# Performance work log

Measured on AMD Instinct MI355X. Metric: run time of the kernel, lower is better.

The kernel has to match this reference:

```python
import jax, jax.numpy as jnp
import numpy as np

_EPS = 1e-5

def _bn(x, g, t, m, v):
    # inference-mode BatchNorm (channels-last)
    return g * (x - m) * jax.lax.rsqrt(v + _EPS) + t

def _lin(x, w, b):
    # 1x1 conv == linear over last (channel) axis; w: (out, in)
    return jnp.einsum('...c,oc->...o', x, w) + b

def _forward(points, k, c0_w, c0_b, c0_g, c0_t, c0_m, c0_v,
             c1_w, c1_b, c1_g, c1_t, c1_m, c1_v,
             a0_w, a0_b, a0_g, a0_t, a0_m, a0_v,
             a1_w, a1_b, a1_g, a1_t, a1_m, a1_v,
             a2_w, a2_b, a2_g, a2_t, a2_m, a2_v,
             c2_w, c2_b, c2_g, c2_t, c2_m, c2_v,
             c3_w, c3_b, c3_g, c3_t, c3_m, c3_v,
             c4_w, c4_b):
    B, N, _ = points.shape
    # per-point MLP: 3 -> 64 -> 64
    x = jax.nn.relu(_bn(_lin(points, c0_w, c0_b), c0_g, c0_t, c0_m, c0_v))
    x = jax.nn.relu(_bn(_lin(x, c1_w, c1_b), c1_g, c1_t, c1_m, c1_v))
    # kNN via squared distances (same ordering as cdist); idx: (B,N,k)
    sq = jnp.sum(points * points, axis=-1)  # (B,N)
    d = sq[:, :, None] + sq[:, None, :] - 2.0 * jnp.einsum('bnc,bmc->bnm', points, points)
    idx = jax.lax.top_k(-d, k)[1]  # (B,N,k) smallest distances
    bidx = jnp.arange(B)[:, None, None]
    grouped_xyz = points[bidx, idx] - points[:, :, None, :]  # (B,N,k,3), centered
    grouped_pts = x[bidx, idx]                                # (B,N,k,64)
    g = jnp.concatenate([grouped_xyz, grouped_pts], axis=-1)  # (B,N,k,67)
    # per-neighbor MLP 67 -> 64 -> 128 -> 128
    for (w, b, ga, t, m, v) in ((a0_w, a0_b, a0_g, a0_t, a0_m, a0_v),
                                (a1_w, a1_b, a1_g, a1_t, a1_m, a1_v),
                                (a2_w, a2_b, a2_g, a2_t, a2_m, a2_v)):
        g = jax.nn.relu(_bn(_lin(g, w, b), ga, t, m, v))
    local = jnp.max(g, axis=2)                 # (B,N,128) max over k neighbors
    gf = jnp.max(local, axis=1, keepdims=True)  # (B,1,128) global feature
    feat = jnp.concatenate([local, jnp.broadcast_to(gf, local.shape)], axis=-1)  # (B,N,256)
    feat = jax.nn.relu(_bn(_lin(feat, c2_w, c2_b), c2_g, c2_t, c2_m, c2_v))
    feat = jax.nn.relu(_bn(_lin(feat, c3_w, c3_b), c3_g, c3_t, c3_m, c3_v))
    # dropout is identity in eval mode
    return _lin(feat, c4_w, c4_b)  # (B,N,6)

def setup_inputs() -> dict:
    key = jax.random.key(0)
    B, N, K = 8, 4096, 16
    specs = [("c0", 64, 3, True), ("c1", 64, 64, True), ("a0", 64, 67, True),
             ("a1", 128, 64, True), ("a2", 128, 128, True), ("c2", 256, 256, True),
             ("c3", 128, 256, True), ("c4", 6, 128, False)]
    inp = {"points": jax.random.normal(key, (B, N, 3), jnp.float32)}
    i = 0
    for name, o, c, has_bn in specs:
        i += 1
        kw = jax.random.fold_in(key, i)
        inp[name + "_w"] = jax.random.normal(kw, (o, c), jnp.float32) * 0.05
        inp[name + "_b"] = jnp.zeros((o,), jnp.float32)
        if has_bn:
            inp[name + "_g"] = jnp.ones((o,), jnp.float32)
            inp[name + "_t"] = jnp.zeros((o,), jnp.float32)
            inp[name + "_m"] = jax.random.normal(jax.random.fold_in(kw, 1), (o,), jnp.float32) * 0.05
            inp[name + "_v"] = jnp.ones((o,), jnp.float32)
    inp["k"] = K
    return inp

def reference(points, c0_w, c0_b, c0_g, c0_t, c0_m, c0_v,
              c1_w, c1_b, c1_g, c1_t, c1_m, c1_v,
              a0_w, a0_b, a0_g, a0_t, a0_m, a0_v,
              a1_w, a1_b, a1_g, a1_t, a1_m, a1_v,
              a2_w, a2_b, a2_g, a2_t, a2_m, a2_v,
              c2_w, c2_b, c2_g, c2_t, c2_m, c2_v,
              c3_w, c3_b, c3_g, c3_t, c3_m, c3_v,
              c4_w, c4_b, k):
    return _forward(points, k, c0_w, c0_b, c0_g, c0_t, c0_m, c0_v,
                    c1_w, c1_b, c1_g, c1_t, c1_m, c1_v,
                    a0_w, a0_b, a0_g, a0_t, a0_m, a0_v,
                    a1_w, a1_b, a1_g, a1_t, a1_m, a1_v,
                    a2_w, a2_b, a2_g, a2_t, a2_m, a2_v,
                    c2_w, c2_b, c2_g, c2_t, c2_m, c2_v,
                    c3_w, c3_b, c3_g, c3_t, c3_m, c3_v,
                    c4_w, c4_b)
```

## Files before the change

### kernel.cpp

```cpp
#include <hip/hip_runtime.h>
#include <math.h>


#define EPSBN 1e-5f

typedef _Float16 v8h  __attribute__((ext_vector_type(8)));
typedef _Float16 v4h  __attribute__((ext_vector_type(4)));
typedef float    v16f __attribute__((ext_vector_type(16)));

#define W0T_OFF   0
#define B0_OFF    192
#define W1T_OFF   256
#define B1_OFF    4352
#define A0XT_OFF  4416
#define A0FT_OFF  4608
#define BA0_OFF   8704
#define A1T_OFF   8768
#define BA1_OFF   16960
#define A2T_OFF   17088
#define BA2_OFF   33472
#define C2T_OFF   33600
#define C3H_OFF   66368
#define BC2_OFF   99136
#define BC3_OFF   132160
#define C4T_OFF   132288
#define BC4_OFF   133056
#define PTS4_OFF  133120
#define Q_OFF     264192
#define C_OFF     2361344
#define IDX_OFF   4458496
#define LOCAL_OFF 4982784
#define GF_OFF    9177088

__device__ __forceinline__ void fold_one(int e, const float* w, const float* b,
    const float* g, const float* t, const float* m, const float* v,
    float* wt, float* bo, int O, int Cfull, int cbeg)
{
    int o = e % O, c = e / O;
    float s = 1.0f;
    if (g) s = g[o] * (1.0f / sqrtf(v[o] + EPSBN));
    wt[c * O + o] = w[o * Cfull + cbeg + c] * s;
    if (c == 0 && bo) {
        float bias = b[o];
        if (g) bias = (bias - m[o]) * s + t[o];
        bo[o] = bias;
    }
}

__global__ __launch_bounds__(256) void fold_kernel(
    const float* c0w, const float* c0b, const float* c0g, const float* c0t, const float* c0m, const float* c0v,
    const float* c1w, const float* c1b, const float* c1g, const float* c1t, const float* c1m, const float* c1v,
    const float* a0w, const float* a0b, const float* a0g, const float* a0t, const float* a0m, const float* a0v,
    const float* a1w, const float* a1b, const float* a1g, const float* a1t, const float* a1m, const float* a1v,
    const float* a2w, const float* a2b, const float* a2g, const float* a2t, const float* a2m, const float* a2v,
    const float* c2w, const float* c2b, const float* c2g, const float* c2t, const float* c2m, const float* c2v,
    const float* c3w, const float* c3b, const float* c3g, const float* c3t, const float* c3m, const float* c3v,
    const float* c4w, const float* c4b,
    float* ws)
{
    int e = blockIdx.x * 256 + threadIdx.x;
    if (e < 192)        { fold_one(e,          c0w, c0b, c0g, c0t, c0m, c0v, ws + W0T_OFF,  ws + B0_OFF,  64, 3,   0); return; }
    e -= 192;
    if (e < 4096)       { fold_one(e,          c1w, c1b, c1g, c1t, c1m, c1v, ws + W1T_OFF,  ws + B1_OFF,  64, 64,  0); return; }
    e -= 4096;
    if (e < 192)        { fold_one(e,          a0w, a0b, a0g, a0t, a0m, a0v, ws + A0XT_OFF, ws + BA0_OFF, 64, 67,  0); return; }
    e -= 192;
    if (e < 4096)       { fold_one(e,          a0w, a0b, a0g, a0t, a0m, a0v, ws + A0FT_OFF, nullptr,      64, 67,  3); return; }
    e -= 4096;
    if (e < 8192) {
        int j = e & 7, l = (e >> 3) & 63, kf = (e >> 9) & 3, wv = e >> 11;
        int o = wv * 32 + (l & 31);
        int c = kf * 16 + (l >> 5) * 8 + j;
        float s = a1g[o] * (1.0f / sqrtf(a1v[o] + EPSBN));
        ((_Float16*)(ws + A1T_OFF))[e] = (_Float16)(a1w[o * 64 + c] * s);
        if (c == 0) ws[BA1_OFF + o] = (a1b[o] - a1m[o]) * s + a1t[o];
        return;
    }
    e -= 8192;
    if (e < 16384) {
        int j = e & 7, l = (e >> 3) & 63, kf = (e >> 9) & 7, wv = e >> 12;
        int o = wv * 32 + (l & 31);
        int c = kf * 16 + (l >> 5) * 8 + j;
        float s = a2g[o] * (1.0f / sqrtf(a2v[o] + EPSBN));
        ((_Float16*)(ws + A2T_OFF))[e] = (_Float16)(a2w[o * 128 + c] * s);
        if (c == 0) ws[BA2_OFF + o] = (a2b[o] - a2m[o]) * s + a2t[o];
        return;
    }
    e -= 16384;
    if (e < 65536) {
        int j = e & 7, l = (e >> 3) & 63, s5 = (e >> 9) & 15, ot = e >> 13;
        int o = ot * 32 + (l & 31);
        int c = s5 * 16 + (l >> 5) * 8 + j;
        float sc = c2g[o] * (1.0f / sqrtf(c2v[o] + EPSBN));
        ((_Float16*)(ws + C2T_OFF))[e] = (_Float16)(c2w[o * 256 + c] * sc);
        if (c == 0) ws[BC2_OFF + o] = (c2b[o] - c2m[o]) * sc + c2t[o];
        return;
    }
    e -= 65536;
    if (e < 32768) {
        int j = e & 7, l = (e >> 3) & 63, s5 = (e >> 9) & 15, ot = e >> 13;
        int o = ot * 32 + (l & 31);
        int c = s5 * 16 + (l >> 5) * 8 + j;
        float sc = c3g[o] * (1.0f / sqrtf(c3v[o] + EPSBN));
        ((_Float16*)(ws + C3H_OFF))[e] = (_Float16)(c3w[o * 256 + c] * sc);
        if (c == 0) ws[BC3_OFF + o] = (c3b[o] - c3m[o]) * sc + c3t[o];
        return;
    }
    e -= 32768;
    if (e < 768)        { fold_one(e,          c4w, c4b, nullptr, nullptr, nullptr, nullptr, ws + C4T_OFF, ws + BC4_OFF, 6, 128, 0); return; }
    e -= 768;
    if (e < 1024)       { ws[GF_OFF + e] = 0.0f; return; }
}

__global__ __launch_bounds__(256) void point_mlp_kernel(const float* __restrict__ pts, float* __restrict__ ws)
{
    __shared__ float sh[4][64][4];
    __shared__ float sx[4][64][4];
    int lane = threadIdx.x & 63;
    int wv = threadIdx.x >> 6;
    int pid0 = blockIdx.x * 16 + wv * 4;

    const float* pc = pts + (size_t)pid0 * 3;
    float c0x = pc[0], c0y = pc[1],  c0z = pc[2];
    float c1x = pc[3], c1y = pc[4],  c1z = pc[5];
    float c2x = pc[6], c2y = pc[7],  c2z = pc[8];
    float c3x = pc[9], c3y = pc[10], c3z = pc[11];

    if (lane < 4) {
        const float* pp = pts + (size_t)(pid0 + lane) * 3;
        float xx = pp[0], yy = pp[1], zz = pp[2];
        float sq = __fadd_rn(__fadd_rn(__fmul_rn(xx, xx), __fmul_rn(yy, yy)), __fmul_rn(zz, zz));
        ((float4*)(ws + PTS4_OFF))[pid0 + lane] = make_float4(xx, yy, zz, sq);
    }

    const float* W0T  = ws + W0T_OFF;
    const float* B0   = ws + B0_OFF;
    const float* W1T  = ws + W1T_OFF;
    const float* B1   = ws + B1_OFF;
    const float* A0XT = ws + A0XT_OFF;
    const float* A0FT = ws + A0FT_OFF;
    const float* BA0  = ws + BA0_OFF;

    float b0 = B0[lane];
    float w0a = W0T[lane], w0b = W0T[64 + lane], w0c = W0T[128 + lane];
    float4 h;
    h.x = fmaxf(fmaf(c0z, w0c, fmaf(c0y, w0b, fmaf(c0x, w0a, b0))), 0.0f);
    h.y = fmaxf(fmaf(c1z, w0c, fmaf(c1y, w0b, fmaf(c1x, w0a, b0))), 0.0f);
    h.z = fmaxf(fmaf(c2z, w0c, fmaf(c2y, w0b, fmaf(c2x, w0a, b0))), 0.0f);
    h.w = fmaxf(fmaf(c3z, w0c, fmaf(c3y, w0b, fmaf(c3x, w0a, b0))), 0.0f);
    *(float4*)&sh[wv][lane][0] = h;

    float b1v = B1[lane];
    float a0 = b1v, a1 = b1v, a2 = b1v, a3 = b1v;
    #pragma unroll 8
    for (int c = 0; c < 64; ++c) {
        float w = W1T[c * 64 + lane];
        float4 hv = *(const float4*)&sh[wv][c][0];
        a0 = fmaf(w, hv.x, a0);
        a1 = fmaf(w, hv.y, a1);
        a2 = fmaf(w, hv.z, a2);
        a3 = fmaf(w, hv.w, a3);
    }
    float4 xv;
    xv.x = fmaxf(a0, 0.0f);
    xv.y = fmaxf(a1, 0.0f);
    xv.z = fmaxf(a2, 0.0f);
    xv.w = fmaxf(a3, 0.0f);
    *(float4*)&sx[wv][lane][0] = xv;

    float ax = A0XT[lane], ay = A0XT[64 + lane], az = A0XT[128 + lane];
    float q0 = __fmul_rn(c0x, ax); q0 = fmaf(c0y, ay, q0); q0 = fmaf(c0z, az, q0);
    float q1 = __fmul_rn(c1x, ax); q1 = fmaf(c1y, ay, q1); q1 = fmaf(c1z, az, q1);
    float q2 = __fmul_rn(c2x, ax); q2 = fmaf(c2y, ay, q2); q2 = fmaf(c2z, az, q2);
    float q3 = __fmul_rn(c3x, ax); q3 = fmaf(c3y, ay, q3); q3 = fmaf(c3z, az, q3);
    ws[Q_OFF + (size_t)(pid0 + 0) * 64 + lane] = q0;
    ws[Q_OFF + (size_t)(pid0 + 1) * 64 + lane] = q1;
    ws[Q_OFF + (size_t)(pid0 + 2) * 64 + lane] = q2;
    ws[Q_OFF + (size_t)(pid0 + 3) * 64 + lane] = q3;

    float ba = BA0[lane];
    float e0 = q0 + ba, e1 = q1 + ba, e2 = q2 + ba, e3 = q3 + ba;
    #pragma unroll 8
    for (int c = 0; c < 64; ++c) {
        float w = A0FT[c * 64 + lane];
        float4 sv = *(const float4*)&sx[wv][c][0];
        e0 = fmaf(w, sv.x, e0);
        e1 = fmaf(w, sv.y, e1);
        e2 = fmaf(w, sv.z, e2);
        e3 = fmaf(w, sv.w, e3);
    }
    ws[C_OFF + (size_t)(pid0 + 0) * 64 + lane] = e0;
    ws[C_OFF + (size_t)(pid0 + 1) * 64 + lane] = e1;
    ws[C_OFF + (size_t)(pid0 + 2) * 64 + lane] = e2;
    ws[C_OFF + (size_t)(pid0 + 3) * 64 + lane] = e3;
}

__device__ __forceinline__ float dist2_ref(float xn, float yn, float zn, float sqn, float4 pm)
{
    float dot = __fmul_rn(xn, pm.x);
    dot = __fmaf_rn(yn, pm.y, dot);
    dot = __fmaf_rn(zn, pm.z, dot);
    float s = __fadd_rn(sqn, pm.w);
    return __fmaf_rn(-2.0f, dot, s);
}

__device__ __forceinline__ float dtilde(float xn, float yn, float zn, float4 pm)
{
    float dot = __fmul_rn(xn, pm.x);
    dot = __fmaf_rn(yn, pm.y, dot);
    dot = __fmaf_rn(zn, pm.z, dot);
    return __fmaf_rn(-2.0f, dot, pm.w);
}

#define KNN_CAP 64
#define KNN_MARGIN 1e-3f

__device__ __forceinline__ void knn_row(
    const float4* __restrict__ pts4, int* __restrict__ IDX,
    float* __restrict__ bufdW, int* __restrict__ bufiW, int* __restrict__ cntp,
    int base, int rbase, int rw, int l, float gm, float tvd)
{
    unsigned long long qm = __ballot(gm <= tvd);

    float4 pr = pts4[rbase + rw];
    float xr = pr.x, yr = pr.y, zr = pr.z, sr = pr.w;
    float tve = __fadd_rn(sr, tvd);

    int cr = 0;
    #define KNN_PROC(GG, CV)                                                   \
    {                                                                          \
        float d = dist2_ref(xr, yr, zr, sr, (CV));                             \
        bool p = (d <= tve);                                                   \
        unsigned long long mk = __ballot(p);                                   \
        int my = __builtin_amdgcn_mbcnt_hi((unsigned)(mk >> 32),               \
                 __builtin_amdgcn_mbcnt_lo((unsigned)mk, 0));                  \
        int slot = cr + my;                                                    \
        if (p && slot < KNN_CAP) { bufdW[slot] = d; bufiW[slot] = (GG) * 64 + l; } \
        cr += (int)__popcll(mk);                                               \
    }
    while (qm) {
        int g0 = __ffsll((unsigned long long)qm) - 1; qm &= qm - 1;
        int g1 = -1, g2 = -1, g3 = -1;
        if (qm) { g1 = __ffsll((unsigned long long)qm) - 1; qm &= qm - 1;
            if (qm) { g2 = __ffsll((unsigned long long)qm) - 1; qm &= qm - 1;
                if (qm) { g3 = __ffsll((unsigned long long)qm) - 1; qm &= qm - 1; } } }
        float4 cv0 = pts4[base + g0 * 64 + l];
        float4 cv1, cv2, cv3;
        if (g1 >= 0) cv1 = pts4[base + g1 * 64 + l];
        if (g2 >= 0) cv2 = pts4[base + g2 * 64 + l];
        if (g3 >= 0) cv3 = pts4[base + g3 * 64 + l];
        KNN_PROC(g0, cv0);
        if (g1 >= 0) KNN_PROC(g1, cv1);
        if (g2 >= 0) KNN_PROC(g2, cv2);
        if (g3 >= 0) KNN_PROC(g3, cv3);
    }
    #undef KNN_PROC
    if (l == 0) *cntp = cr;

    if (cr <= KNN_CAP) {
        unsigned long long key = ~0ULL;
        if (l < cr) {
            unsigned u = __float_as_uint(bufdW[l]);
            u = (u & 0x80000000u) ? ~u : (u | 0x80000000u);
            key = ((unsigned long long)u << 32) | (unsigned)bufiW[l];
        }
        if (cr <= 32) {
            #pragma unroll
            for (int k = 2; k <= 32; k <<= 1) {
                #pragma unroll
                for (int j = k >> 1; j > 0; j >>= 1) {
                    unsigned long long o = __shfl_xor(key, j);
                    bool mx = (((l & j) != 0) == ((l & k) == 0));
                    key = mx ? (key > o ? key : o) : (key < o ? key : o);
                }
            }
        } else {
            #pragma unroll
            for (int k = 2; k <= 64; k <<= 1) {
                #pragma unroll
                for (int j = k >> 1; j > 0; j >>= 1) {
                    unsigned long long o = __shfl_xor(key, j);
                    bool mx = (((l & j) != 0) == ((l & k) == 0));
                    key = mx ? (key > o ? key : o) : (key < o ? key : o);
                }
            }
        }
        if (l < 16)
            IDX[(rbase + rw) * 16 + l] = (int)(key & 0xFFFFFFFFu);
    }
}

__global__ __launch_bounds__(1024) void knn_kernel(float* __restrict__ ws)
{
    __shared__ float gmins[64 * 65];
    __shared__ float bufd[16][72];
    __shared__ int   bufi[16][72];
    __shared__ int   cnt[64];

    const float4* __restrict__ pts4 = (const float4*)(ws + PTS4_OFF);
    int* IDX = (int*)(ws + IDX_OFF);

    const int l     = threadIdx.x & 63;
    const int row   = l;
    const int wvu   = __builtin_amdgcn_readfirstlane(threadIdx.x >> 6);
    const int base  = (blockIdx.x >> 6) << 12;
    const int rbase = blockIdx.x * 64;
    const int r     = rbase + row;

    float4 pn = pts4[r];
    float xn = pn.x, yn = pn.y, zn = pn.z;

    #pragma unroll
    for (int g = 0; g < 4; ++g) {
        const float4* __restrict__ cp = pts4 + base + wvu * 256 + g * 64;
        float mn0 = INFINITY, mn1 = INFINITY, mn2 = INFINITY, mn3 = INFINITY;
        #pragma unroll 4
        for (int i = 0; i < 64; i += 4) {
            mn0 = fminf(mn0, dtilde(xn, yn, zn, cp[i + 0]));
            mn1 = fminf(mn1, dtilde(xn, yn, zn, cp[i + 1]));
            mn2 = fminf(mn2, dtilde(xn, yn, zn, cp[i + 2]));
            mn3 = fminf(mn3, dtilde(xn, yn, zn, cp[i + 3]));
        }
        gmins[row * 65 + wvu * 4 + g] = fminf(fminf(mn0, mn1), fminf(mn2, mn3));
    }
    __syncthreads();

    float gm0 = gmins[(wvu * 4 + 0) * 65 + l];
    float gm1 = gmins[(wvu * 4 + 1) * 65 + l];
    float gm2 = gmins[(wvu * 4 + 2) * 65 + l];
    float gm3 = gmins[(wvu * 4 + 3) * 65 + l];
    float v0 = gm0, v1 = gm1, v2 = gm2, v3 = gm3;
    #pragma unroll
    for (int k = 2; k <= 64; k <<= 1) {
        #pragma unroll
        for (int j = k >> 1; j > 0; j >>= 1) {
            float o0 = __shfl_xor(v0, j);
            float o1 = __shfl_xor(v1, j);
            float o2 = __shfl_xor(v2, j);
            float o3 = __shfl_xor(v3, j);
            bool mx = (((l & j) != 0) == ((l & k) == 0));
            v0 = mx ? fmaxf(v0, o0) : fminf(v0, o0);
            v1 = mx ? fmaxf(v1, o1) : fminf(v1, o1);
            v2 = mx ? fmaxf(v2, o2) : fminf(v2, o2);
            v3 = mx ? fmaxf(v3, o3) : fminf(v3, o3);
        }
    }
    float tvd0 = __shfl(v0, 16) + KNN_MARGIN;
    float tvd1 = __shfl(v1, 16) + KNN_MARGIN;
    float tvd2 = __shfl(v2, 16) + KNN_MARGIN;
    float tvd3 = __shfl(v3, 16) + KNN_MARGIN;

    knn_row(pts4, IDX, bufd[wvu], bufi[wvu], &cnt[wvu * 4 + 0], base, rbase, wvu * 4 + 0, l, gm0, tvd0);
    knn_row(pts4, IDX, bufd[wvu], bufi[wvu], &cnt[wvu * 4 + 1], base, rbase, wvu * 4 + 1, l, gm1, tvd1);
    knn_row(pts4, IDX, bufd[wvu], bufi[wvu], &cnt[wvu * 4 + 2], base, rbase, wvu * 4 + 2, l, gm2, tvd2);
    knn_row(pts4, IDX, bufd[wvu], bufi[wvu], &cnt[wvu * 4 + 3], base, rbase, wvu * 4 + 3, l, gm3, tvd3);
    __syncthreads();

    if (threadIdx.x < 64 && cnt[threadIdx.x] > KNN_CAP) {
        int* out = IDX + (rbase + threadIdx.x) * 16;
        float4 pq = pts4[rbase + threadIdx.x];
        float hd[16]; int hi[16];
        #pragma unroll
        for (int t2 = 0; t2 < 16; ++t2) { hd[t2] = INFINITY; hi[t2] = 0; }
        for (int mm = 0; mm < 4096; ++mm) {
            float d = dist2_ref(pq.x, pq.y, pq.z, pq.w, pts4[base + mm]);
            if (d < hd[15]) {
                float vd = d; int vi = mm;
                #pragma unroll
                for (int t2 = 0; t2 < 16; ++t2) {
                    bool sm = vd < hd[t2];
                    float td = hd[t2]; int ti = hi[t2];
                    if (sm) { hd[t2] = vd; hi[t2] = vi; vd = td; vi = ti; }
                }
            }
        }
        for (int jj = 0; jj < 16; ++jj) out[jj] = hi[jj];
    }
}

__device__ __forceinline__ void nbr_stage_g1(
    _Float16* sG1, const float* Cf, const float* Qf,
    int t, int gpt0, int g, int base, int m)
{
    int r = t >> 2, cs = t & 3;
    int gpt = gpt0 + g * 4 + (r >> 4);
    const float4* crow = (const float4*)(Cf + (size_t)(base + m) * 64) + cs * 4;
    const float4* qrow = (const float4*)(Qf + (size_t)gpt * 64) + cs * 4;
    v8h h0, h1;
    #pragma unroll
    for (int u = 0; u < 2; ++u) {
        float4 cv = crow[u], qv = qrow[u];
        h0[u * 4 + 0] = (_Float16)fmaxf(cv.x - qv.x, 0.0f);
        h0[u * 4 + 1] = (_Float16)fmaxf(cv.y - qv.y, 0.0f);
        h0[u * 4 + 2] = (_Float16)fmaxf(cv.z - qv.z, 0.0f);
        h0[u * 4 + 3] = (_Float16)fmaxf(cv.w - qv.w, 0.0f);
    }
    #pragma unroll
    for (int u = 0; u < 2; ++u) {
        float4 cv = crow[2 + u], qv = qrow[2 + u];
        h1[u * 4 + 0] = (_Float16)fmaxf(cv.x - qv.x, 0.0f);
        h1[u * 4 + 1] = (_Float16)fmaxf(cv.y - qv.y, 0.0f);
        h1[u * 4 + 2] = (_Float16)fmaxf(cv.z - qv.z, 0.0f);
        h1[u * 4 + 3] = (_Float16)fmaxf(cv.w - qv.w, 0.0f);
    }
    int rs = r & 7;
    *(v8h*)&sG1[r * 64 + ((cs * 2    ) ^ rs) * 8] = h0;
    *(v8h*)&sG1[r * 64 + ((cs * 2 + 1) ^ rs) * 8] = h1;
}

__global__ __launch_bounds__(256) void nbr_mlp_mfma_kernel(float* __restrict__ ws)
{
    __shared__ __align__(16) unsigned char smem[33280];
    _Float16* sG1   = (_Float16*)smem;
    _Float16* sH1   = (_Float16*)(smem + 8192);
    float*    sPool = (float*)(smem + 24576);
    float*    sB1   = (float*)(smem + 32768);

    const int t   = threadIdx.x;
    const int l   = t & 63;
    const int w   = t >> 6;
    const int ln  = l & 31;
    const int hi  = l >> 5;
    const int blk = blockIdx.x;
    const int gpt0 = blk * 16;
    const int base = (blk >> 8) << 12;

    const float* Cf = ws + C_OFF;
    const float* Qf = ws + Q_OFF;
    const int* IDX = (const int*)(ws + IDX_OFF);

    if (t < 128) sB1[t] = ws[BA1_OFF + t];
    float b2ch = ws[BA2_OFF + w * 32 + ln];

    int mi[4];
    {
        int r = t >> 2;
        #pragma unroll
        for (int g = 0; g < 4; ++g)
            mi[g] = IDX[(gpt0 + g * 4 + (r >> 4)) * 16 + (r & 15)];
    }

    v8h fa[4], fa2[8];
    {
        const float4* a1img = (const float4*)(ws + A1T_OFF);
        const float4* a2img = (const float4*)(ws + A2T_OFF);
        #pragma unroll
        for (int kf = 0; kf < 4; ++kf) {
            float4 tmp = a1img[(w * 4 + kf) * 64 + l];
            fa[kf] = *(v8h*)&tmp;
        }
        #pragma unroll
        for (int kf = 0; kf < 8; ++kf) {
            float4 tmp = a2img[(w * 8 + kf) * 64 + l];
            fa2[kf] = *(v8h*)&tmp;
        }
    }

    nbr_stage_g1(sG1, Cf, Qf, t, gpt0, 0, base, mi[0]);
    __syncthreads();

    for (int g = 0; g < 4; ++g) {
        #pragma unroll
        for (int rt = 0; rt < 2; ++rt) {
            int r = rt * 32 + ln, rs = r & 7;
            v16f acc;
            #pragma unroll
            for (int i = 0; i < 16; ++i) acc[i] = 0.0f;
            #pragma unroll
            for (int kf = 0; kf < 4; ++kf) {
                v8h fb = *(const v8h*)&sG1[r * 64 + ((kf * 2 + hi) ^ rs) * 8];
                acc = __builtin_amdgcn_mfma_f32_32x32x16_f16(fa[kf], fb, acc, 0, 0, 0);
            }
            #pragma unroll
            for (int q = 0; q < 4; ++q) {
                float4 b4 = *(const float4*)&sB1[w * 32 + 8 * q + 4 * hi];
                v4h hv;
                hv[0] = (_Float16)fmaxf(acc[q * 4 + 0] + b4.x, 0.0f);
                hv[1] = (_Float16)fmaxf(acc[q * 4 + 1] + b4.y, 0.0f);
                hv[2] = (_Float16)fmaxf(acc[q * 4 + 2] + b4.z, 0.0f);
                hv[3] = (_Float16)fmaxf(acc[q * 4 + 3] + b4.w, 0.0f);
                int gg = w * 4 + q;
                *(v4h*)&sH1[r * 128 + ((gg ^ rs) * 8) + 4 * hi] = hv;
            }
        }
        __syncthreads();

        if (g < 3) nbr_stage_g1(sG1, Cf, Qf, t, gpt0, g + 1, base, mi[g + 1]);

        #pragma unroll
        for (int rt = 0; rt < 2; ++rt) {
            int r = rt * 32 + ln, rs = r & 7;
            v16f acc;
            #pragma unroll
            for (int i = 0; i < 16; ++i) acc[i] = 0.0f;
            #pragma unroll
            for (int kf = 0; kf < 8; ++kf) {
                v8h fb = *(const v8h*)&sH1[r * 128 + ((kf * 2 + hi) ^ rs) * 8];
                acc = __builtin_amdgcn_mfma_f32_32x32x16_f16(fb, fa2[kf], acc, 0, 0, 0);
            }
            float p0 = acc[0], p1 = acc[8];
            #pragma unroll
            for (int i = 1; i < 8; ++i) { p0 = fmaxf(p0, acc[i]); p1 = fmaxf(p1, acc[8 + i]); }
            p0 = fmaxf(p0, __shfl_xor(p0, 32));
            p1 = fmaxf(p1, __shfl_xor(p1, 32));
            float o0 = fmaxf(p0 + b2ch, 0.0f);
            float o1 = fmaxf(p1 + b2ch, 0.0f);
            if (hi == 0) {
                int p = g * 4 + rt * 2;
                sPool[p * 128 + w * 32 + ln]       = o0;
                sPool[(p + 1) * 128 + w * 32 + ln] = o1;
            }
        }
        __syncthreads();
    }

    {
        float* LOCAL = ws + LOCAL_OFF;
        const float4* sp4 = (const float4*)sPool;
        #pragma unroll
        for (int u = 0; u < 2; ++u) {
            int e = t + 256 * u;
            int pp = e >> 5, cc = e & 31;
            ((float4*)&LOCAL[(size_t)(gpt0 + pp) * 128])[cc] = sp4[e];
        }
    }

    if (t < 128) {
        float m = 0.0f;
        #pragma unroll
        for (int p = 0; p < 16; ++p) m = fmaxf(m, sPool[p * 128 + t]);
        atomicMax((int*)(ws + GF_OFF) + (blk >> 8) * 128 + t, __float_as_int(m));
    }
}

__global__ __launch_bounds__(256) void head_mfma_kernel(float* __restrict__ ws, float* __restrict__ out)
{
    __shared__ __align__(16) unsigned char smem[66560];
    _Float16* sF  = (_Float16*)smem;
    float*    sF3 = (float*)smem;
    _Float16* sF2 = (_Float16*)(smem + 33792);

    const int t  = threadIdx.x;
    const int l  = t & 63;
    const int w  = t >> 6;
    const int ln = l & 31;
    const int hi = l >> 5;
    const int gpt0 = blockIdx.x * 64;
    const int b = blockIdx.x >> 6;

    const float4* c2h = (const float4*)(ws + C2T_OFF);
    const float4* c3h = (const float4*)(ws + C3H_OFF);

    {
        int m = t >> 2, cs = t & 3;
        const float4* src = (cs < 2)
            ? (const float4*)(ws + LOCAL_OFF + (size_t)(gpt0 + m) * 128) + cs * 16
            : (const float4*)(ws + GF_OFF + b * 128) + (cs - 2) * 16;
        int c0 = cs * 64;
        #pragma unroll
        for (int u = 0; u < 8; ++u) {
            float4 a0 = src[u * 2], a1 = src[u * 2 + 1];
            v8h h;
            h[0] = (_Float16)a0.x; h[1] = (_Float16)a0.y;
            h[2] = (_Float16)a0.z; h[3] = (_Float16)a0.w;
            h[4] = (_Float16)a1.x; h[5] = (_Float16)a1.y;
            h[6] = (_Float16)a1.z; h[7] = (_Float16)a1.w;
            int g = ((c0 >> 3) + u) ^ (m & 31);
            *(v8h*)&sF[m * 256 + g * 8] = h;
        }
    }
    __syncthreads();

    #pragma unroll
    for (int ot = 0; ot < 2; ++ot) {
        int ot2 = 2 * w + ot;
        v8h fa[16];
        #pragma unroll
        for (int s = 0; s < 16; ++s) {
            float4 tmp = c2h[(ot2 * 16 + s) * 64 + l];
            fa[s] = *(v8h*)&tmp;
        }
        float b2[16];
        #pragma unroll
        for (int i = 0; i < 16; ++i)
            b2[i] = ws[BC2_OFF + ot2 * 32 + (i & 3) + 8 * (i >> 2) + 4 * hi];
        #pragma unroll
        for (int mt = 0; mt < 2; ++mt) {
            int m = mt * 32 + ln;
            v16f acc;
            #pragma unroll
            for (int i = 0; i < 16; ++i) acc[i] = 0.0f;
            #pragma unroll
            for (int s = 0; s < 16; ++s) {
                v8h fb = *(const v8h*)&sF[m * 256 + (((2 * s + hi) ^ ln) * 8)];
                acc = __builtin_amdgcn_mfma_f32_32x32x16_f16(fa[s], fb, acc, 0, 0, 0);
            }
            #pragma unroll
            for (int q = 0; q < 4; ++q) {
                v4h hv;
                #pragma unroll
                for (int j = 0; j < 4; ++j)
                    hv[j] = (_Float16)fmaxf(acc[q * 4 + j] + b2[q * 4 + j], 0.0f);
                *(v4h*)&sF2[m * 256 + (((ot2 * 4 + q) ^ ln) * 8) + 4 * hi] = hv;
            }
        }
    }
    __syncthreads();

    {
        v8h fa[16];
        #pragma unroll
        for (int s = 0; s < 16; ++s) {
            float4 tmp = c3h[(w * 16 + s) * 64 + l];
            fa[s] = *(v8h*)&tmp;
        }
        float b3[16];
        #pragma unroll
        for (int i = 0; i < 16; ++i)
            b3[i] = ws[BC3_OFF + w * 32 + (i & 3) + 8 * (i >> 2) + 4 * hi];
        #pragma unroll
        for (int mt = 0; mt < 2; ++mt) {
            int m = mt * 32 + ln;
            v16f acc;
            #pragma unroll
            for (int i = 0; i < 16; ++i) acc[i] = 0.0f;
            #pragma unroll
            for (int s = 0; s < 16; ++s) {
                v8h fb = *(const v8h*)&sF2[m * 256 + (((2 * s + hi) ^ ln) * 8)];
                acc = __builtin_amdgcn_mfma_f32_32x32x16_f16(fa[s], fb, acc, 0, 0, 0);
            }
            #pragma unroll
            for (int q = 0; q < 4; ++q) {
                float4 hv;
                hv.x = fmaxf(acc[q * 4 + 0] + b3[q * 4 + 0], 0.0f);
                hv.y = fmaxf(acc[q * 4 + 1] + b3[q * 4 + 1], 0.0f);
                hv.z = fmaxf(acc[q * 4 + 2] + b3[q * 4 + 2], 0.0f);
                hv.w = fmaxf(acc[q * 4 + 3] + b3[q * 4 + 3], 0.0f);
                *(float4*)&sF3[m * 132 + w * 32 + q * 8 + 4 * hi] = hv;
            }
        }
    }
    __syncthreads();

    const float* C4T = ws + C4T_OFF;
    for (int mo = t; mo < 384; mo += 256) {
        int m = mo / 6, o = mo - m * 6;
        float a = ws[BC4_OFF + o];
        const float4* f4 = (const float4*)(sF3 + m * 132);
        #pragma unroll 8
        for (int kq = 0; kq < 32; ++kq) {
            float4 f = f4[kq];
            a = fmaf(f.x, C4T[(kq * 4 + 0) * 6 + o], a);
            a = fmaf(f.y, C4T[(kq * 4 + 1) * 6 + o], a);
            a = fmaf(f.z, C4T[(kq * 4 + 2) * 6 + o], a);
            a = fmaf(f.w, C4T[(kq * 4 + 3) * 6 + o], a);
        }
        out[(size_t)(gpt0 + m) * 6 + o] = a;
    }
}

extern "C" void kernel_launch(void* const* d_in, const int* in_sizes, int n_in,
                              void* d_out, int out_size, void* d_ws, size_t ws_size,
                              hipStream_t stream)
{
    const float* pts = (const float*)d_in[0];
    float* ws = (float*)d_ws;
    float* out = (float*)d_out;

    fold_kernel<<<521, 256, 0, stream>>>(
        (const float*)d_in[1],  (const float*)d_in[2],  (const float*)d_in[3],  (const float*)d_in[4],  (const float*)d_in[5],  (const float*)d_in[6],
        (const float*)d_in[7],  (const float*)d_in[8],  (const float*)d_in[9],  (const float*)d_in[10], (const float*)d_in[11], (const float*)d_in[12],
        (const float*)d_in[13], (const float*)d_in[14], (const float*)d_in[15], (const float*)d_in[16], (const float*)d_in[17], (const float*)d_in[18],
        (const float*)d_in[19], (const float*)d_in[20], (const float*)d_in[21], (const float*)d_in[22], (const float*)d_in[23], (const float*)d_in[24],
        (const float*)d_in[25], (const float*)d_in[26], (const float*)d_in[27], (const float*)d_in[28], (const float*)d_in[29], (const float*)d_in[30],
        (const float*)d_in[31], (const float*)d_in[32], (const float*)d_in[33], (const float*)d_in[34], (const float*)d_in[35], (const float*)d_in[36],
        (const float*)d_in[37], (const float*)d_in[38], (const float*)d_in[39], (const float*)d_in[40], (const float*)d_in[41], (const float*)d_in[42],
        (const float*)d_in[43], (const float*)d_in[44],
        ws);

    point_mlp_kernel<<<2048, 256, 0, stream>>>(pts, ws);
    knn_kernel<<<512, 1024, 0, stream>>>(ws);
    nbr_mlp_mfma_kernel<<<2048, 256, 0, stream>>>(ws);
    head_mfma_kernel<<<512, 256, 0, stream>>>(ws, out);
}
```

Measured before the change: 291.6 us.

## Interleave two kNN rows per wave and widen head kernel to 512 threads

The kNN candidate scan now handles two query rows at once per wave. It interleaves their candidate-group loads and the ballot/compaction steps, and runs both bitonic sorts together, to expose more memory- and instruction-level parallelism. Each row gets its own shared-memory buffer, which increases LDS usage. Separately, the head kernel moves from 256 to 512 threads, giving each wave one output tile per GEMM stage. This gives more waves to hide latency but means less register reuse of weights per wave.

New measurement: 283.5 us, median of 2. 2.8% less time.

```diff
diff --git a/kernel.cpp b/kernel.cpp
--- a/kernel.cpp
+++ b/kernel.cpp
@@ -215,86 +215,100 @@
 #define KNN_CAP 64
 #define KNN_MARGIN 1e-3f
 
-__device__ __forceinline__ void knn_row(
+__device__ __forceinline__ void knn_pair(
     const float4* __restrict__ pts4, int* __restrict__ IDX,
-    float* __restrict__ bufdW, int* __restrict__ bufiW, int* __restrict__ cntp,
-    int base, int rbase, int rw, int l, float gm, float tvd)
-{
-    unsigned long long qm = __ballot(gm <= tvd);
-
-    float4 pr = pts4[rbase + rw];
-    float xr = pr.x, yr = pr.y, zr = pr.z, sr = pr.w;
-    float tve = __fadd_rn(sr, tvd);
-
-    int cr = 0;
-    #define KNN_PROC(GG, CV)                                                   \
+    float* __restrict__ bdA, int* __restrict__ biA,
+    float* __restrict__ bdB, int* __restrict__ biB,
+    int* __restrict__ cntA, int* __restrict__ cntB,
+    int base, int rgA, int rgB, int l,
+    float gmA, float gmB, float tvdA, float tvdB)
+{
+    float4 pA = pts4[rgA];
+    float4 pB = pts4[rgB];
+    float tveA = __fadd_rn(pA.w, tvdA);
+    float tveB = __fadd_rn(pB.w, tvdB);
+    unsigned long long qA = __ballot(gmA <= tvdA);
+    unsigned long long qB = __ballot(gmB <= tvdB);
+    int crA = 0, crB = 0;
+
+    #define KNN_PROC2(GG, CV, PP, TVE, CR, BD, BI)                             \
     {                                                                          \
-        float d = dist2_ref(xr, yr, zr, sr, (CV));                             \
-        bool p = (d <= tve);                                                   \
+        float d = dist2_ref((PP).x, (PP).y, (PP).z, (PP).w, (CV));             \
+        bool p = ((GG) >= 0) & (d <= (TVE));                                   \
         unsigned long long mk = __ballot(p);                                   \
         int my = __builtin_amdgcn_mbcnt_hi((unsigned)(mk >> 32),               \
                  __builtin_amdgcn_mbcnt_lo((unsigned)mk, 0));                  \
-        int slot = cr + my;                                                    \
-        if (p && slot < KNN_CAP) { bufdW[slot] = d; bufiW[slot] = (GG) * 64 + l; } \
-        cr += (int)__popcll(mk);                                               \
-    }
-    while (qm) {
-        int g0 = __ffsll((unsigned long long)qm) - 1; qm &= qm - 1;
-        int g1 = -1, g2 = -1, g3 = -1;
-        if (qm) { g1 = __ffsll((unsigned long long)qm) - 1; qm &= qm - 1;
-            if (qm) { g2 = __ffsll((unsigned long long)qm) - 1; qm &= qm - 1;
-                if (qm) { g3 = __ffsll((unsigned long long)qm) - 1; qm &= qm - 1; } } }
-        float4 cv0 = pts4[base + g0 * 64 + l];
-        float4 cv1, cv2, cv3;
-        if (g1 >= 0) cv1 = pts4[base + g1 * 64 + l];
-        if (g2 >= 0) cv2 = pts4[base + g2 * 64 + l];
-        if (g3 >= 0) cv3 = pts4[base + g3 * 64 + l];
-        KNN_PROC(g0, cv0);
-        if (g1 >= 0) KNN_PROC(g1, cv1);
-        if (g2 >= 0) KNN_PROC(g2, cv2);
-        if (g3 >= 0) KNN_PROC(g3, cv3);
-    }
-    #undef KNN_PROC
-    if (l == 0) *cntp = cr;
-
-    if (cr <= KNN_CAP) {
-        unsigned long long key = ~0ULL;
-        if (l < cr) {
-            unsigned u = __float_as_uint(bufdW[l]);
-            u = (u & 0x80000000u) ? ~u : (u | 0x80000000u);
-            key = ((unsigned long long)u << 32) | (unsigned)bufiW[l];
-        }
-        if (cr <= 32) {
-            #pragma unroll
-            for (int k = 2; k <= 32; k <<= 1) {
-                #pragma unroll
-                for (int j = k >> 1; j > 0; j >>= 1) {
-                    unsigned long long o = __shfl_xor(key, j);
-                    bool mx = (((l & j) != 0) == ((l & k) == 0));
-                    key = mx ? (key > o ? key : o) : (key < o ? key : o);
-                }
-            }
-        } else {
-            #pragma unroll
-            for (int k = 2; k <= 64; k <<= 1) {
-                #pragma unroll
-                for (int j = k >> 1; j > 0; j >>= 1) {
-                    unsigned long long o = __shfl_xor(key, j);
-                    bool mx = (((l & j) != 0) == ((l & k) == 0));
-                    key = mx ? (key > o ? key : o) : (key < o ? key : o);
-                }
-            }
-        }
-        if (l < 16)
-            IDX[(rbase + rw) * 16 + l] = (int)(key & 0xFFFFFFFFu);
-    }
-}
-
-__global__ __launch_bounds__(1024) void knn_kernel(float* __restrict__ ws)
+        int slot = (CR) + my;                                                  \
+        if (p && slot < KNN_CAP) { (BD)[slot] = d; (BI)[slot] = (GG) * 64 + l; } \
+        (CR) += (int)__popcll(mk);                                             \
+    }
+    while (qA | qB) {
+        int a0 = -1, a1 = -1, b0 = -1, b1 = -1;
+        if (qA) { a0 = __ffsll((unsigned long long)qA) - 1; qA &= qA - 1;
+            if (qA) { a1 = __ffsll((unsigned long long)qA) - 1; qA &= qA - 1; } }
+        if (qB) { b0 = __ffsll((unsigned long long)qB) - 1; qB &= qB - 1;
+            if (qB) { b1 = __ffsll((unsigned long long)qB) - 1; qB &= qB - 1; } }
+        float4 ca0, ca1, cb0, cb1;
+        if (a0 >= 0) ca0 = pts4[base + a0 * 64 + l];
+        if (b0 >= 0) cb0 = pts4[base + b0 * 64 + l];
+        if (a1 >= 0) ca1 = pts4[base + a1 * 64 + l];
+        if (b1 >= 0) cb1 = pts4[base + b1 * 64 + l];
+        KNN_PROC2(a0, ca0, pA, tveA, crA, bdA, biA);
+        KNN_PROC2(b0, cb0, pB, tveB, crB, bdB, biB);
+        KNN_PROC2(a1, ca1, pA, tveA, crA, bdA, biA);
+        KNN_PROC2(b1, cb1, pB, tveB, crB, bdB, biB);
+    }
+    #undef KNN_PROC2
+    if (l == 0) { *cntA = crA; *cntB = crB; }
+
+    unsigned long long kA = ~0ULL, kB = ~0ULL;
+    if (l < crA) {
+        unsigned u = __float_as_uint(bdA[l]);
+        u = (u & 0x80000000u) ? ~u : (u | 0x80000000u);
+        kA = ((unsigned long long)u << 32) | (unsigned)biA[l];
+    }
+    if (l < crB) {
+        unsigned u = __float_as_uint(bdB[l]);
+        u = (u & 0x80000000u) ? ~u : (u | 0x80000000u);
+        kB = ((unsigned long long)u << 32) | (unsigned)biB[l];
+    }
+    int crm = crA > crB ? crA : crB;
+    if (crm <= 32) {
+        #pragma unroll
+        for (int k = 2; k <= 32; k <<= 1) {
+            #pragma unroll
+            for (int j = k >> 1; j > 0; j >>= 1) {
+                unsigned long long oA = __shfl_xor(kA, j);
+                unsigned long long oB = __shfl_xor(kB, j);
+                bool mx = (((l & j) != 0) == ((l & k) == 0));
+                kA = mx ? (kA > oA ? kA : oA) : (kA < oA ? kA : oA);
+                kB = mx ? (kB > oB ? kB : oB) : (kB < oB ? kB : oB);
+            }
+        }
+    } else {
+        #pragma unroll
+        for (int k = 2; k <= 64; k <<= 1) {
+            #pragma unroll
+            for (int j = k >> 1; j > 0; j >>= 1) {
+                unsigned long long oA = __shfl_xor(kA, j);
+                unsigned long long oB = __shfl_xor(kB, j);
+                bool mx = (((l & j) != 0) == ((l & k) == 0));
+                kA = mx ? (kA > oA ? kA : oA) : (kA < oA ? kA : oA);
+                kB = mx ? (kB > oB ? kB : oB) : (kB < oB ? kB : oB);
+            }
+        }
+    }
+    if (l < 16) {
+        if (crA <= KNN_CAP) IDX[rgA * 16 + l] = (int)(kA & 0xFFFFFFFFu);
+        if (crB <= KNN_CAP) IDX[rgB * 16 + l] = (int)(kB & 0xFFFFFFFFu);
+    }
+}
+
+__global__ __launch_bounds__(1024, 8) void knn_kernel(float* __restrict__ ws)
 {
     __shared__ float gmins[64 * 65];
-    __shared__ float bufd[16][72];
-    __shared__ int   bufi[16][72];
+    __shared__ float bufd[16][4][72];
+    __shared__ int   bufi[16][4][72];
     __shared__ int   cnt[64];
 
     const float4* __restrict__ pts4 = (const float4*)(ws + PTS4_OFF);
@@ -350,10 +364,12 @@
     float tvd2 = __shfl(v2, 16) + KNN_MARGIN;
     float tvd3 = __shfl(v3, 16) + KNN_MARGIN;
 
-    knn_row(pts4, IDX, bufd[wvu], bufi[wvu], &cnt[wvu * 4 + 0], base, rbase, wvu * 4 + 0, l, gm0, tvd0);
-    knn_row(pts4, IDX, bufd[wvu], bufi[wvu], &cnt[wvu * 4 + 1], base, rbase, wvu * 4 + 1, l, gm1, tvd1);
-    knn_row(pts4, IDX, bufd[wvu], bufi[wvu], &cnt[wvu * 4 + 2], base, rbase, wvu * 4 + 2, l, gm2, tvd2);
-    knn_row(pts4, IDX, bufd[wvu], bufi[wvu], &cnt[wvu * 4 + 3], base, rbase, wvu * 4 + 3, l, gm3, tvd3);
+    knn_pair(pts4, IDX, &bufd[wvu][0][0], &bufi[wvu][0][0], &bufd[wvu][1][0], &bufi[wvu][1][0],
+             &cnt[wvu * 4 + 0], &cnt[wvu * 4 + 1], base,
+             rbase + wvu * 4 + 0, rbase + wvu * 4 + 1, l, gm0, gm1, tvd0, tvd1);
+    knn_pair(pts4, IDX, &bufd[wvu][2][0], &bufi[wvu][2][0], &bufd[wvu][3][0], &bufi[wvu][3][0],
+             &cnt[wvu * 4 + 2], &cnt[wvu * 4 + 3], base,
+             rbase + wvu * 4 + 2, rbase + wvu * 4 + 3, l, gm2, gm3, tvd2, tvd3);
     __syncthreads();
 
     if (threadIdx.x < 64 && cnt[threadIdx.x] > KNN_CAP) {
@@ -533,7 +549,7 @@
     }
 }
 
-__global__ __launch_bounds__(256) void head_mfma_kernel(float* __restrict__ ws, float* __restrict__ out)
+__global__ __launch_bounds__(512) void head_mfma_kernel(float* __restrict__ ws, float* __restrict__ out)
 {
     __shared__ __align__(16) unsigned char smem[66560];
     _Float16* sF  = (_Float16*)smem;
@@ -552,38 +568,36 @@
     const float4* c3h = (const float4*)(ws + C3H_OFF);
 
     {
-        int m = t >> 2, cs = t & 3;
-        const float4* src = (cs < 2)
-            ? (const float4*)(ws + LOCAL_OFF + (size_t)(gpt0 + m) * 128) + cs * 16
-            : (const float4*)(ws + GF_OFF + b * 128) + (cs - 2) * 16;
-        int c0 = cs * 64;
-        #pragma unroll
-        for (int u = 0; u < 8; ++u) {
+        int m = t >> 3, cs = t & 7;
+        const float4* src = (cs < 4)
+            ? (const float4*)(ws + LOCAL_OFF + (size_t)(gpt0 + m) * 128) + cs * 8
+            : (const float4*)(ws + GF_OFF + b * 128) + (cs - 4) * 8;
+        int gbase = cs * 4;
+        #pragma unroll
+        for (int u = 0; u < 4; ++u) {
             float4 a0 = src[u * 2], a1 = src[u * 2 + 1];
             v8h h;
             h[0] = (_Float16)a0.x; h[1] = (_Float16)a0.y;
             h[2] = (_Float16)a0.z; h[3] = (_Float16)a0.w;
             h[4] = (_Float16)a1.x; h[5] = (_Float16)a1.y;
             h[6] = (_Float16)a1.z; h[7] = (_Float16)a1.w;
-            int g = ((c0 >> 3) + u) ^ (m & 31);
+            int g = (gbase + u) ^ (m & 31);
             *(v8h*)&sF[m * 256 + g * 8] = h;
         }
     }
     __syncthreads();
 
-    #pragma unroll
-    for (int ot = 0; ot < 2; ++ot) {
-        int ot2 = 2 * w + ot;
+    {
         v8h fa[16];
         #pragma unroll
         for (int s = 0; s < 16; ++s) {
-            float4 tmp = c2h[(ot2 * 16 + s) * 64 + l];
+            float4 tmp = c2h[(w * 16 + s) * 64 + l];
             fa[s] = *(v8h*)&tmp;
         }
         float b2[16];
         #pragma unroll
         for (int i = 0; i < 16; ++i)
-            b2[i] = ws[BC2_OFF + ot2 * 32 + (i & 3) + 8 * (i >> 2) + 4 * hi];
+            b2[i] = ws[BC2_OFF + w * 32 + (i & 3) + 8 * (i >> 2) + 4 * hi];
         #pragma unroll
         for (int mt = 0; mt < 2; ++mt) {
             int m = mt * 32 + ln;
@@ -601,49 +615,47 @@
                 #pragma unroll
                 for (int j = 0; j < 4; ++j)
                     hv[j] = (_Float16)fmaxf(acc[q * 4 + j] + b2[q * 4 + j], 0.0f);
-                *(v4h*)&sF2[m * 256 + (((ot2 * 4 + q) ^ ln) * 8) + 4 * hi] = hv;
+                *(v4h*)&sF2[m * 256 + (((w * 4 + q) ^ ln) * 8) + 4 * hi] = hv;
             }
         }
     }
     __syncthreads();
 
     {
+        int tw = w >> 1, mt = w & 1;
         v8h fa[16];
         #pragma unroll
         for (int s = 0; s < 16; ++s) {
-            float4 tmp = c3h[(w * 16 + s) * 64 + l];
+            float4 tmp = c3h[(tw * 16 + s) * 64 + l];
             fa[s] = *(v8h*)&tmp;
         }
         float b3[16];
         #pragma unroll
         for (int i = 0; i < 16; ++i)
-            b3[i] = ws[BC3_OFF + w * 32 + (i & 3) + 8 * (i >> 2) + 4 * hi];
-        #pragma unroll
-        for (int mt = 0; mt < 2; ++mt) {
-            int m = mt * 32 + ln;
-            v16f acc;
-            #pragma unroll
-            for (int i = 0; i < 16; ++i) acc[i] = 0.0f;
-            #pragma unroll
-            for (int s = 0; s < 16; ++s) {
-                v8h fb = *(const v8h*)&sF2[m * 256 + (((2 * s + hi) ^ ln) * 8)];
-                acc = __builtin_amdgcn_mfma_f32_32x32x16_f16(fa[s], fb, acc, 0, 0, 0);
-            }
-            #pragma unroll
-            for (int q = 0; q < 4; ++q) {
-                float4 hv;
-                hv.x = fmaxf(acc[q * 4 + 0] + b3[q * 4 + 0], 0.0f);
-                hv.y = fmaxf(acc[q * 4 + 1] + b3[q * 4 + 1], 0.0f);
-                hv.z = fmaxf(acc[q * 4 + 2] + b3[q * 4 + 2], 0.0f);
-                hv.w = fmaxf(acc[q * 4 + 3] + b3[q * 4 + 3], 0.0f);
-                *(float4*)&sF3[m * 132 + w * 32 + q * 8 + 4 * hi] = hv;
-            }
+            b3[i] = ws[BC3_OFF + tw * 32 + (i & 3) + 8 * (i >> 2) + 4 * hi];
+        int m = mt * 32 + ln;
+        v16f acc;
+        #pragma unroll
+        for (int i = 0; i < 16; ++i) acc[i] = 0.0f;
+        #pragma unroll
+        for (int s = 0; s < 16; ++s) {
+            v8h fb = *(const v8h*)&sF2[m * 256 + (((2 * s + hi) ^ ln) * 8)];
+            acc = __builtin_amdgcn_mfma_f32_32x32x16_f16(fa[s], fb, acc, 0, 0, 0);
+        }
+        #pragma unroll
+        for (int q = 0; q < 4; ++q) {
+            float4 hv;
+            hv.x = fmaxf(acc[q * 4 + 0] + b3[q * 4 + 0], 0.0f);
+            hv.y = fmaxf(acc[q * 4 + 1] + b3[q * 4 + 1], 0.0f);
+            hv.z = fmaxf(acc[q * 4 + 2] + b3[q * 4 + 2], 0.0f);
+            hv.w = fmaxf(acc[q * 4 + 3] + b3[q * 4 + 3], 0.0f);
+            *(float4*)&sF3[m * 132 + tw * 32 + q * 8 + 4 * hi] = hv;
         }
     }
     __syncthreads();
 
     const float* C4T = ws + C4T_OFF;
-    for (int mo = t; mo < 384; mo += 256) {
+    for (int mo = t; mo < 384; mo += 512) {
         int m = mo / 6, o = mo - m * 6;
         float a = ws[BC4_OFF + o];
         const float4* f4 = (const float4*)(sF3 + m * 132);
@@ -681,5 +693,5 @@
     point_mlp_kernel<<<2048, 256, 0, stream>>>(pts, ws);
     knn_kernel<<<512, 1024, 0, stream>>>(ws);
     nbr_mlp_mfma_kernel<<<2048, 256, 0, stream>>>(ws);
-    head_mfma_kernel<<<512, 256, 0, stream>>>(ws, out);
-}
+    head_mfma_kernel<<<512, 512, 0, stream>>>(ws, out);
+}
```
